# Kernel tuning notes

Hardware: AMD Instinct MI355X
Metric: run time of the kernel (lower is better)

## Reference

```python
import jax, jax.numpy as jnp
import numpy as np

NUM_OBJ = 32
OBJ_DIM = 128
MSG_W = 256
FIN_W = 256
BATCH = 256
BN_EPS = 1e-5
NEG_SLOPE = 0.01


def _linear_init(key, fan_in, fan_out):
    # torch nn.Linear default: U(-1/sqrt(fan_in), 1/sqrt(fan_in))
    kw, kb = jax.random.split(key)
    bound = 1.0 / np.sqrt(fan_in)
    w = jax.random.uniform(kw, (fan_out, fan_in), jnp.float32, -bound, bound)
    b = jax.random.uniform(kb, (fan_out,), jnp.float32, -bound, bound)
    return w, b


def setup_inputs() -> dict:
    key = jax.random.key(0)
    ks = jax.random.split(key, 8)
    state = jax.random.normal(ks[0], (BATCH, NUM_OBJ, OBJ_DIM), jnp.float32)
    edges = jax.random.randint(ks[1], (BATCH, NUM_OBJ * NUM_OBJ), 0, 2).astype(jnp.float32)
    msg_w1, msg_b1 = _linear_init(ks[2], OBJ_DIM * 2, MSG_W)
    msg_w2, msg_b2 = _linear_init(ks[3], MSG_W, OBJ_DIM)
    fin_w1, fin_b1 = _linear_init(ks[4], OBJ_DIM * 2, FIN_W)
    fin_w2, fin_b2 = _linear_init(ks[5], FIN_W, OBJ_DIM)
    msg_gamma = jnp.ones((MSG_W,), jnp.float32)
    msg_beta = jnp.zeros((MSG_W,), jnp.float32)
    fin_gamma = jnp.ones((FIN_W,), jnp.float32)
    fin_beta = jnp.zeros((FIN_W,), jnp.float32)
    return {
        "state": state, "edges": edges,
        "msg_w1": msg_w1, "msg_b1": msg_b1, "msg_gamma": msg_gamma, "msg_beta": msg_beta,
        "msg_w2": msg_w2, "msg_b2": msg_b2,
        "fin_w1": fin_w1, "fin_b1": fin_b1, "fin_gamma": fin_gamma, "fin_beta": fin_beta,
        "fin_w2": fin_w2, "fin_b2": fin_b2,
    }


def _batchnorm_train(x, gamma, beta):
    # training-mode BatchNorm1d: batch stats over rows, biased variance
    mean = jnp.mean(x, axis=0)
    var = jnp.mean(jnp.square(x - mean), axis=0)
    return (x - mean) * jax.lax.rsqrt(var + BN_EPS) * gamma + beta


def _mlp(x, w1, b1, gamma, beta, w2, b2):
    h = x @ w1.T + b1
    h = _batchnorm_train(h, gamma, beta)
    h = jnp.where(h >= 0, h, NEG_SLOPE * h)  # LeakyReLU
    return h @ w2.T + b2


def reference(state, edges, msg_w1, msg_b1, msg_gamma, msg_beta, msg_w2, msg_b2,
              fin_w1, fin_b1, fin_gamma, fin_beta, fin_w2, fin_b2):
    B, n, d = state.shape
    src = jnp.repeat(jnp.arange(n), n)   # [n*n]
    tgt = jnp.tile(jnp.arange(n), n)     # [n*n]
    sources = state[:, src]              # [B, n*n, d]
    targets = state[:, tgt]              # [B, n*n, d]
    e = edges[:, :, None]                # [B, n*n, 1]
    need = jnp.concatenate([sources * e, targets * e], axis=2)  # [B, n*n, 2d]
    msgs = _mlp(need.reshape(-1, 2 * d), msg_w1, msg_b1, msg_gamma, msg_beta, msg_w2, msg_b2)
    agg = jnp.sum(msgs.reshape(B, n, n, d), axis=2)  # sum over inner edge group
    sm = jnp.concatenate([state, agg], axis=2).reshape(-1, 2 * d)
    out = _mlp(sm, fin_w1, fin_b1, fin_gamma, fin_beta, fin_w2, fin_b2)
    return out.reshape(B, n, d)
```

## Files before the change

kernel.cpp:

```cpp
#include <hip/hip_runtime.h>

#define NOBJ   32
#define DIM    128
#define HW     256
#define R1     8192
#define NPAIR  262144
#define BN_EPS 1e-5f

typedef unsigned short u16;
typedef unsigned int   u32;
typedef __attribute__((ext_vector_type(8))) short bf16x8;
typedef __attribute__((ext_vector_type(4))) float f32x4;
typedef __attribute__((ext_vector_type(4))) unsigned short u16x4;
typedef __attribute__((ext_vector_type(4))) unsigned int u32x4;

__device__ __forceinline__ u16 f2bf(float f) {
    union { float f; unsigned u; } v; v.f = f;
    unsigned r = v.u + 0x7fffu + ((v.u >> 16) & 1u);
    return (u16)(r >> 16);
}
__device__ __forceinline__ float bf2f(u16 u) {
    union { unsigned u; float f; } v; v.u = ((unsigned)u) << 16; return v.f;
}
__device__ __forceinline__ u16x4 cvt4(float4 v) {
    u16x4 r;
    r[0] = f2bf(v.x); r[1] = f2bf(v.y); r[2] = f2bf(v.z); r[3] = f2bf(v.w);
    return r;
}
__device__ __forceinline__ bf16x8 cvt8_f32(const float* p) {
    f32x4 v0 = *(const f32x4*)p, v1 = *(const f32x4*)(p + 4);
    bf16x8 r;
    #pragma unroll
    for (int k = 0; k < 4; ++k) {
        r[k]     = (short)f2bf(v0[k]);
        r[4 + k] = (short)f2bf(v1[k]);
    }
    return r;
}
__device__ __forceinline__ bf16x8 cvt8_bn_b(const u16* p, const float* a, const float* d) {
    u16x4 v0 = *(const u16x4*)p, v1 = *(const u16x4*)(p + 4);
    f32x4 a0 = *(const f32x4*)a, a1 = *(const f32x4*)(a + 4);
    f32x4 d0 = *(const f32x4*)d, d1 = *(const f32x4*)(d + 4);
    bf16x8 r;
    #pragma unroll
    for (int k = 0; k < 4; ++k) {
        float x0 = fmaf(a0[k], bf2f(v0[k]), d0[k]); x0 = fmaxf(x0, 0.01f * x0);
        float x1 = fmaf(a1[k], bf2f(v1[k]), d1[k]); x1 = fmaxf(x1, 0.01f * x1);
        r[k]     = (short)f2bf(x0);
        r[4 + k] = (short)f2bf(x1);
    }
    return r;
}

__global__ __launch_bounds__(256) void prep_kernel(
    const float* __restrict__ w1, const float4* __restrict__ w2,
    const float4* __restrict__ fw1, const float4* __restrict__ fw2,
    u16x4* __restrict__ W1b, u16x4* __restrict__ W2b,
    u16x4* __restrict__ FW1b, u16x4* __restrict__ FW2b,
    f32x4* __restrict__ sums)
{
    int g = blockIdx.x * 256 + threadIdx.x;
    if (g < 16384) {
        const int o = g * 4, n = o >> 7, k = o & 127;
        const float4 v = *(const float4*)(w1 + (n < 256 ? n * 256 + k
                                                        : (n - 256) * 256 + 128 + k));
        W1b[g] = cvt4(v); return;
    }
    g -= 16384;
    if (g < 8192) { W2b[g] = cvt4(w2[g]); return; }
    g -= 8192;
    if (g < 16384) { FW1b[g] = cvt4(fw1[g]); return; }
    g -= 16384;
    if (g < 8192) { FW2b[g] = cvt4(fw2[g]); return; }
    g -= 8192;
    if (g < 264) { const f32x4 z = {}; sums[g] = z; }
}

__global__ __launch_bounds__(1024) void pq_stats(
    const float* __restrict__ state, const u16* __restrict__ W1b,
    const float* __restrict__ edges, const float* __restrict__ b1,
    u16* __restrict__ PQb, u16* __restrict__ Ab, float* __restrict__ EQf,
    float* __restrict__ sums)
{
    __shared__ float Qls[33 * 256];
    __shared__ float redA[16 * 256];
    __shared__ float redB[16 * 256];
    __shared__ u32 masks[32];
    __shared__ __align__(16) unsigned char list8[32 * 32];
    __shared__ float cdf[32];

    const int b    = blockIdx.x;
    const int t    = threadIdx.x;
    const int lane = t & 63;
    const int w    = t >> 6;
    const int lr   = lane & 15;
    const int lk   = (lane >> 4) * 8;
    const int c0   = lane * 4;

    if (t < 256) ((u32*)list8)[t] = 0x20202020u;
    if (t < 64) { const f32x4 z = {}; *(f32x4*)&Qls[32 * 256 + t * 4] = z; }

    const float ev = edges[(size_t)b * 1024 + t];

    const int col0 = w * 32;
    f32x4 acc[2][2] = {};
    #pragma unroll
    for (int ks = 0; ks < 4; ++ks) {
        const int kabs = ks * 32 + lk;
        bf16x8 af[2];
        #pragma unroll
        for (int rf = 0; rf < 2; ++rf)
            af[rf] = cvt8_f32(state + (size_t)(b * 32 + rf * 16 + lr) * 128 + kabs);
        if (w == 0) {
            #pragma unroll
            for (int rf = 0; rf < 2; ++rf)
                *(bf16x8*)(Ab + (size_t)(b * 32 + rf * 16 + lr) * 128 + kabs) = af[rf];
        }
        #pragma unroll
        for (int cf = 0; cf < 2; ++cf) {
            const bf16x8 bf = *(const bf16x8*)(W1b + (size_t)(col0 + cf * 16 + lr) * 128 + kabs);
            #pragma unroll
            for (int rf = 0; rf < 2; ++rf)
                acc[rf][cf] = __builtin_amdgcn_mfma_f32_16x16x32_bf16(af[rf], bf, acc[rf][cf], 0, 0, 0);
        }
    }
    #pragma unroll
    for (int rf = 0; rf < 2; ++rf)
        #pragma unroll
        for (int cf = 0; cf < 2; ++cf) {
            const int col = col0 + cf * 16 + lr;
            #pragma unroll
            for (int r = 0; r < 4; ++r) {
                const int row = rf * 16 + (lane >> 4) * 4 + r;
                const u16 u = f2bf(acc[rf][cf][r]);
                PQb[(size_t)(b * 32 + row) * 512 + col] = u;
                if (col >= 256) Qls[row * 256 + (col - 256)] = bf2f(u);
            }
        }
    __syncthreads();

    {
        const int il_t = t >> 5;
        const int j_t  = t & 31;
        const unsigned long long bal = __ballot(ev != 0.f);
        const u32 m32 = (lane < 32) ? (u32)bal : (u32)(bal >> 32);
        if (ev != 0.f)
            list8[il_t * 32 + __popc(m32 & ((1u << j_t) - 1u))] = (unsigned char)j_t;
        if (j_t == 0) masks[il_t] = m32;
    }
    __syncthreads();

    if (t < 32) {
        u32 cnt = 0;
        #pragma unroll
        for (int i = 0; i < 32; ++i) cnt += (masks[i] >> t) & 1u;
        cdf[t] = (float)cnt;
    }
    if (t == 0) {
        int tot = 0;
        #pragma unroll
        for (int i = 0; i < 32; ++i) tot += __popc(masks[i]);
        atomicAdd(&sums[512], (float)tot);
    }

    const f32x4 b14 = *(const f32x4*)(b1 + c0);
    f32x4 sumA = {}, sumB = {};

    #pragma unroll
    for (int ii = 0; ii < 2; ++ii) {
        const int il = 2 * w + ii;
        const int n1 = __popc(masks[il]);
        const int npad = (n1 + 3) & ~3;
        const float frd = (float)n1;
        f32x4 eq = {};
        const u32x4 l0 = *(const u32x4*)(list8 + il * 32);
        const u32x4 l1 = *(const u32x4*)(list8 + il * 32 + 16);
        const u32 wbuf[8] = {l0[0], l0[1], l0[2], l0[3], l1[0], l1[1], l1[2], l1[3]};
        #pragma unroll
        for (int wi = 0; wi < 8; ++wi) {
            if (wi * 4 >= npad) break;
            const u32 w4 = wbuf[wi];
            #pragma unroll
            for (int kb = 0; kb < 4; ++kb) {
                const int j = (w4 >> (kb * 8)) & 0xff;
                const f32x4 q = *(const f32x4*)&Qls[j * 256 + c0];
                #pragma unroll
                for (int k = 0; k < 4; ++k) eq[k] += q[k];
            }
        }
        *(f32x4*)(EQf + (size_t)(b * 32 + il) * 256 + c0) = eq;
        const u16x4 pu = *(const u16x4*)(PQb + (size_t)(b * 32 + il) * 512 + c0);
        #pragma unroll
        for (int k = 0; k < 4; ++k) {
            const float pb = bf2f(pu[k]) + b14[k];
            sumA[k] += frd * pb + eq[k];
            sumB[k] = fmaf(frd * pb + 2.f * eq[k], pb, sumB[k]);
        }
    }
    __syncthreads();

    #pragma unroll
    for (int jj = 0; jj < 2; ++jj) {
        const int j = 2 * w + jj;
        const float cdj = cdf[j];
        const f32x4 q = *(const f32x4*)&Qls[j * 256 + c0];
        #pragma unroll
        for (int k = 0; k < 4; ++k) sumB[k] = fmaf(cdj * q[k], q[k], sumB[k]);
    }
    *(f32x4*)&redA[w * 256 + c0] = sumA;
    *(f32x4*)&redB[w * 256 + c0] = sumB;
    __syncthreads();
    if (t < 256) {
        float a = 0.f, bb = 0.f;
        #pragma unroll
        for (int ww = 0; ww < 16; ++ww) {
            a  += redA[ww * 256 + t];
            bb += redB[ww * 256 + t];
        }
        atomicAdd(&sums[t], a);
        atomicAdd(&sums[256 + t], bb);
    }
}

__global__ __launch_bounds__(512) void s_agg_kernel(
    const u16* __restrict__ PQb, const float* __restrict__ edges,
    const float* __restrict__ EQf, const float* __restrict__ sums,
    const float* __restrict__ gamma, const float* __restrict__ beta,
    const float* __restrict__ b1,
    const u16* __restrict__ W2b, const float* __restrict__ b2,
    u16* __restrict__ aggb)
{
    __shared__ float Qls[33 * 256];
    __shared__ u16 Ssb[16 * 256];
    __shared__ __align__(16) unsigned char list8[16 * 32];
    __shared__ int n1s[16];

    const int b    = blockIdx.x;
    const int i0   = blockIdx.y * 16;
    const int t    = threadIdx.x;
    const int lane = t & 63;
    const int w    = t >> 6;
    const int lr   = lane & 15;
    const int lk   = (lane >> 4) * 8;
    const int c0   = lane * 4;

    const float Etot = sums[512];
    const float nz   = (float)NPAIR - Etot;
    const float invN = 1.f / (float)NPAIR;
    const f32x4 s1  = *(const f32x4*)(sums + c0);
    const f32x4 s2  = *(const f32x4*)(sums + 256 + c0);
    const f32x4 g4  = *(const f32x4*)(gamma + c0);
    const f32x4 be4 = *(const f32x4*)(beta + c0);
    const f32x4 b14 = *(const f32x4*)(b1 + c0);
    f32x4 a4, d4, ld4;
    #pragma unroll
    for (int k = 0; k < 4; ++k) {
        const float mean = (s1[k] + nz * b14[k]) * invN;
        const float ms   = (s2[k] + nz * b14[k] * b14[k]) * invN;
        const float var  = fmaf(-mean, mean, ms);
        a4[k]  = g4[k] * rsqrtf(var + BN_EPS);
        d4[k]  = fmaf(b14[k] - mean, a4[k], be4[k]);
        ld4[k] = fmaxf(d4[k], 0.01f * d4[k]);
    }

    #pragma unroll
    for (int it = 0; it < 4; ++it) {
        const int row = w + it * 8;
        const u16x4 qu = *(const u16x4*)(PQb + (size_t)(b * 32 + row) * 512 + 256 + c0);
        f32x4 q;
        #pragma unroll
        for (int k = 0; k < 4; ++k) q[k] = a4[k] * bf2f(qu[k]);
        *(f32x4*)&Qls[row * 256 + c0] = q;
    }
    if (t < 64) { const f32x4 z = {}; *(f32x4*)&Qls[32 * 256 + t * 4] = z; }
    if (t < 128) ((u32*)list8)[t] = 0x20202020u;

    const float ev = edges[(size_t)b * 1024 + (i0 + (t >> 5)) * 32 + (t & 31)];
    __syncthreads();

    {
        const int il_t = t >> 5;
        const int j_t  = t & 31;
        const unsigned long long bal = __ballot(ev != 0.f);
        const u32 m32 = (lane < 32) ? (u32)bal : (u32)(bal >> 32);
        if (ev != 0.f)
            list8[il_t * 32 + __popc(m32 & ((1u << j_t) - 1u))] = (unsigned char)j_t;
        if (j_t == 0) n1s[il_t] = __popc(m32);
    }
    __syncthreads();

    #pragma unroll
    for (int ii = 0; ii < 2; ++ii) {
        const int il = 2 * w + ii;
        const int gi = b * 32 + i0 + il;
        const int n1 = n1s[il];
        const int npad = (n1 + 3) & ~3;
        const float frd = (float)n1;
        const float fz = (float)(32 - n1);
        const float fp = (float)(npad - n1);
        const u16x4 pu = *(const u16x4*)(PQb + (size_t)gi * 512 + c0);
        const f32x4 eq4 = *(const f32x4*)(EQf + (size_t)gi * 256 + c0);
        f32x4 ap, absacc;
        #pragma unroll
        for (int k = 0; k < 4; ++k) {
            ap[k] = fmaf(a4[k], bf2f(pu[k]), d4[k]);
            absacc[k] = -fp * fabsf(ap[k]);
        }
        const u32x4 l0 = *(const u32x4*)(list8 + il * 32);
        const u32x4 l1 = *(const u32x4*)(list8 + il * 32 + 16);
        const u32 wbuf[8] = {l0[0], l0[1], l0[2], l0[3], l1[0], l1[1], l1[2], l1[3]};
        #pragma unroll
        for (int wi = 0; wi < 8; ++wi) {
            if (wi * 4 >= npad) break;
            const u32 w4 = wbuf[wi];
            #pragma unroll
            for (int kb = 0; kb < 4; ++kb) {
                const int j = (w4 >> (kb * 8)) & 0xff;
                const f32x4 q = *(const f32x4*)&Qls[j * 256 + c0];
                #pragma unroll
                for (int k = 0; k < 4; ++k)
                    absacc[k] += fabsf(ap[k] + q[k]);
            }
        }
        u16x4 o;
        #pragma unroll
        for (int k = 0; k < 4; ++k) {
            const float lin = fmaf(frd, ap[k], a4[k] * eq4[k]);
            const float S = fmaf(fz, ld4[k], fmaf(0.505f, lin, 0.495f * absacc[k]));
            o[k] = f2bf(S);
        }
        const int off = (lane * 8) ^ ((il & 7) << 4);
        *(u16x4*)((char*)Ssb + il * 512 + off) = o;
    }
    __syncthreads();

    const int colw = w * 16;
    f32x4 acc2 = {};
    #pragma unroll
    for (int ks = 0; ks < 8; ++ks) {
        const int rdoff = (ks * 64 + (lane >> 4) * 16) ^ ((lr & 7) << 4);
        const bf16x8 afr = *(const bf16x8*)((const char*)Ssb + lr * 512 + rdoff);
        const bf16x8 bfr = *(const bf16x8*)(W2b + (size_t)(colw + lr) * 256 + ks * 32 + lk);
        acc2 = __builtin_amdgcn_mfma_f32_16x16x32_bf16(afr, bfr, acc2, 0, 0, 0);
    }
    {
        const int col = colw + lr;
        const float bv = (float)NOBJ * b2[col];
        #pragma unroll
        for (int r = 0; r < 4; ++r) {
            const int rowl = (lane >> 4) * 4 + r;
            aggb[(size_t)(b * 32 + i0 + rowl) * 128 + col] = f2bf(acc2[r] + bv);
        }
    }
}

__global__ __launch_bounds__(256) void h2_gemm(
    const u16* __restrict__ Ab, const u16* __restrict__ aggb,
    const u16* __restrict__ FW1b, const float* __restrict__ fb1,
    u16* __restrict__ H2b, float* __restrict__ sums2)
{
    __shared__ float sred[64];
    const int lane = threadIdx.x & 63;
    const int wave = threadIdx.x >> 6;
    const int row0 = blockIdx.y * 64 + wave * 16;
    const int col0 = blockIdx.x * 32;
    const int lr = lane & 15;
    const int lk = (lane >> 4) * 8;

    f32x4 acc[2] = {};
    #pragma unroll
    for (int ks = 0; ks < 8; ++ks) {
        const int kabs = ks * 32 + lk;
        const bf16x8 af = (kabs < 128)
            ? *(const bf16x8*)(Ab   + (size_t)(row0 + lr) * 128 + kabs)
            : *(const bf16x8*)(aggb + (size_t)(row0 + lr) * 128 + (kabs - 128));
        #pragma unroll
        for (int cf = 0; cf < 2; ++cf) {
            const bf16x8 bf = *(const bf16x8*)(FW1b + (size_t)(col0 + cf * 16 + lr) * 256 + kabs);
            acc[cf] = __builtin_amdgcn_mfma_f32_16x16x32_bf16(af, bf, acc[cf], 0, 0, 0);
        }
    }

    if (threadIdx.x < 64) sred[threadIdx.x] = 0.f;
    __syncthreads();
    #pragma unroll
    for (int cf = 0; cf < 2; ++cf) {
        const int col = col0 + cf * 16 + lr;
        const float bv = fb1[col];
        float s = 0.f, ss = 0.f;
        #pragma unroll
        for (int r = 0; r < 4; ++r) {
            const int row = row0 + (lane >> 4) * 4 + r;
            const float v = acc[cf][r] + bv;
            H2b[(size_t)row * 256 + col] = f2bf(v);
            s += v;
            ss = fmaf(v, v, ss);
        }
        atomicAdd(&sred[cf * 16 + lr], s);
        atomicAdd(&sred[32 + cf * 16 + lr], ss);
    }
    __syncthreads();
    if (threadIdx.x < 32) {
        atomicAdd(&sums2[col0 + threadIdx.x], sred[threadIdx.x]);
        atomicAdd(&sums2[256 + col0 + threadIdx.x], sred[32 + threadIdx.x]);
    }
}

__global__ __launch_bounds__(256) void out_gemm(
    const u16* __restrict__ H2b, const u16* __restrict__ FW2b,
    const float* __restrict__ fb2, const float* __restrict__ sums2,
    const float* __restrict__ gamma, const float* __restrict__ beta,
    float* __restrict__ out)
{
    __shared__ float adl[512];
    const int t = threadIdx.x;
    {
        const float invN = 1.f / (float)R1;
        const float mean = sums2[t] * invN;
        const float var  = fmaf(-mean, mean, sums2[256 + t] * invN);
        const float a    = gamma[t] * rsqrtf(var + BN_EPS);
        adl[t]       = a;
        adl[256 + t] = fmaf(-mean, a, beta[t]);
    }
    __syncthreads();

    const int lane = t & 63;
    const int wave = t >> 6;
    const int row0 = blockIdx.y * 64 + wave * 16;
    const int col0 = blockIdx.x * 32;
    const int lr = lane & 15;
    const int lk = (lane >> 4) * 8;

    f32x4 acc[2] = {};
    #pragma unroll
    for (int ks = 0; ks < 8; ++ks) {
        const int kabs = ks * 32 + lk;
        const bf16x8 af = cvt8_bn_b(H2b + (size_t)(row0 + lr) * 256 + kabs,
                                    adl + kabs, adl + 256 + kabs);
        #pragma unroll
        for (int cf = 0; cf < 2; ++cf) {
            const bf16x8 bf = *(const bf16x8*)(FW2b + (size_t)(col0 + cf * 16 + lr) * 256 + kabs);
            acc[cf] = __builtin_amdgcn_mfma_f32_16x16x32_bf16(af, bf, acc[cf], 0, 0, 0);
        }
    }
    #pragma unroll
    for (int cf = 0; cf < 2; ++cf) {
        const int col = col0 + cf * 16 + lr;
        const float bv = fb2[col];
        #pragma unroll
        for (int r = 0; r < 4; ++r) {
            const int row = row0 + (lane >> 4) * 4 + r;
            out[(size_t)row * 128 + col] = acc[cf][r] + bv;
        }
    }
}

extern "C" void kernel_launch(void* const* d_in, const int* in_sizes, int n_in,
                              void* d_out, int out_size, void* d_ws, size_t ws_size,
                              hipStream_t stream)
{
    const float* state     = (const float*)d_in[0];
    const float* edges     = (const float*)d_in[1];
    const float* msg_w1    = (const float*)d_in[2];
    const float* msg_b1    = (const float*)d_in[3];
    const float* msg_gamma = (const float*)d_in[4];
    const float* msg_beta  = (const float*)d_in[5];
    const float* msg_w2    = (const float*)d_in[6];
    const float* msg_b2    = (const float*)d_in[7];
    const float* fin_w1    = (const float*)d_in[8];
    const float* fin_b1    = (const float*)d_in[9];
    const float* fin_gamma = (const float*)d_in[10];
    const float* fin_beta  = (const float*)d_in[11];
    const float* fin_w2    = (const float*)d_in[12];
    const float* fin_b2    = (const float*)d_in[13];

    char* w = (char*)d_ws;
    u16*   PQb  = (u16*)(w);
    u16*   Ab   = (u16*)(w + 8388608);
    u16*   aggb = (u16*)(w + 10485760);
    u16*   H2b  = (u16*)(w + 12582912);
    float* EQf  = (float*)(w + 16777216);
    u16*   W1b  = (u16*)(w + 25165824);
    u16*   W2b  = (u16*)(w + 25296896);
    u16*   FW1b = (u16*)(w + 25362432);
    u16*   FW2b = (u16*)(w + 25493504);
    float* sums = (float*)(w + 25559040);
    float* sums2 = sums + 544;

    prep_kernel<<<195, 256, 0, stream>>>(
        msg_w1, (const float4*)msg_w2, (const float4*)fin_w1, (const float4*)fin_w2,
        (u16x4*)W1b, (u16x4*)W2b, (u16x4*)FW1b, (u16x4*)FW2b, (f32x4*)sums);

    pq_stats<<<256, 1024, 0, stream>>>(state, W1b, edges, msg_b1,
                                       PQb, Ab, EQf, sums);

    s_agg_kernel<<<dim3(256, 2), 512, 0, stream>>>(
        PQb, edges, EQf, sums, msg_gamma, msg_beta, msg_b1, W2b, msg_b2, aggb);

    h2_gemm<<<dim3(8, 128), 256, 0, stream>>>(Ab, aggb, FW1b, fin_b1, H2b, sums2);

    out_gemm<<<dim3(4, 128), 256, 0, stream>>>(
        H2b, FW2b, fin_b2, sums2, fin_gamma, fin_beta, (float*)d_out);
}
```

Baseline: 69.09 us.

## Fuse h2 GEMM into aggregation kernel and drop weight-conversion prep kernel

```diff
diff --git a/kernel.cpp b/kernel.cpp
--- a/kernel.cpp
+++ b/kernel.cpp
@@ -1,9 +1,5 @@
 #include <hip/hip_runtime.h>
 
-#define NOBJ   32
-#define DIM    128
-#define HW     256
-#define R1     8192
 #define NPAIR  262144
 #define BN_EPS 1e-5f
 
@@ -22,11 +18,6 @@
 __device__ __forceinline__ float bf2f(u16 u) {
     union { unsigned u; float f; } v; v.u = ((unsigned)u) << 16; return v.f;
 }
-__device__ __forceinline__ u16x4 cvt4(float4 v) {
-    u16x4 r;
-    r[0] = f2bf(v.x); r[1] = f2bf(v.y); r[2] = f2bf(v.z); r[3] = f2bf(v.w);
-    return r;
-}
 __device__ __forceinline__ bf16x8 cvt8_f32(const float* p) {
     f32x4 v0 = *(const f32x4*)p, v1 = *(const f32x4*)(p + 4);
     bf16x8 r;
@@ -52,34 +43,10 @@
     return r;
 }
 
-__global__ __launch_bounds__(256) void prep_kernel(
-    const float* __restrict__ w1, const float4* __restrict__ w2,
-    const float4* __restrict__ fw1, const float4* __restrict__ fw2,
-    u16x4* __restrict__ W1b, u16x4* __restrict__ W2b,
-    u16x4* __restrict__ FW1b, u16x4* __restrict__ FW2b,
-    f32x4* __restrict__ sums)
-{
-    int g = blockIdx.x * 256 + threadIdx.x;
-    if (g < 16384) {
-        const int o = g * 4, n = o >> 7, k = o & 127;
-        const float4 v = *(const float4*)(w1 + (n < 256 ? n * 256 + k
-                                                        : (n - 256) * 256 + 128 + k));
-        W1b[g] = cvt4(v); return;
-    }
-    g -= 16384;
-    if (g < 8192) { W2b[g] = cvt4(w2[g]); return; }
-    g -= 8192;
-    if (g < 16384) { FW1b[g] = cvt4(fw1[g]); return; }
-    g -= 16384;
-    if (g < 8192) { FW2b[g] = cvt4(fw2[g]); return; }
-    g -= 8192;
-    if (g < 264) { const f32x4 z = {}; sums[g] = z; }
-}
-
 __global__ __launch_bounds__(1024) void pq_stats(
-    const float* __restrict__ state, const u16* __restrict__ W1b,
+    const float* __restrict__ state, const float* __restrict__ w1,
     const float* __restrict__ edges, const float* __restrict__ b1,
-    u16* __restrict__ PQb, u16* __restrict__ Ab, float* __restrict__ EQf,
+    u16* __restrict__ PQb, float* __restrict__ EQf,
     float* __restrict__ sums)
 {
     __shared__ float Qls[33 * 256];
@@ -111,17 +78,15 @@
         #pragma unroll
         for (int rf = 0; rf < 2; ++rf)
             af[rf] = cvt8_f32(state + (size_t)(b * 32 + rf * 16 + lr) * 128 + kabs);
-        if (w == 0) {
+        #pragma unroll
+        for (int cf = 0; cf < 2; ++cf) {
+            const int coln = col0 + cf * 16 + lr;
+            const float* wp = (coln < 256) ? (w1 + (size_t)coln * 256 + kabs)
+                                           : (w1 + (size_t)(coln - 256) * 256 + 128 + kabs);
+            const bf16x8 bfr = cvt8_f32(wp);
             #pragma unroll
             for (int rf = 0; rf < 2; ++rf)
-                *(bf16x8*)(Ab + (size_t)(b * 32 + rf * 16 + lr) * 128 + kabs) = af[rf];
-        }
-        #pragma unroll
-        for (int cf = 0; cf < 2; ++cf) {
-            const bf16x8 bf = *(const bf16x8*)(W1b + (size_t)(col0 + cf * 16 + lr) * 128 + kabs);
-            #pragma unroll
-            for (int rf = 0; rf < 2; ++rf)
-                acc[rf][cf] = __builtin_amdgcn_mfma_f32_16x16x32_bf16(af[rf], bf, acc[rf][cf], 0, 0, 0);
+                acc[rf][cf] = __builtin_amdgcn_mfma_f32_16x16x32_bf16(af[rf], bfr, acc[rf][cf], 0, 0, 0);
         }
     }
     #pragma unroll
@@ -222,18 +187,22 @@
     }
 }
 
-__global__ __launch_bounds__(512) void s_agg_kernel(
+__global__ __launch_bounds__(512) void s_agg_h2_kernel(
     const u16* __restrict__ PQb, const float* __restrict__ edges,
     const float* __restrict__ EQf, const float* __restrict__ sums,
     const float* __restrict__ gamma, const float* __restrict__ beta,
-    const float* __restrict__ b1,
-    const u16* __restrict__ W2b, const float* __restrict__ b2,
-    u16* __restrict__ aggb)
+    const float* __restrict__ b1, const float* __restrict__ state,
+    const float* __restrict__ w2, const float* __restrict__ b2,
+    const float* __restrict__ fw1, const float* __restrict__ fb1,
+    u16* __restrict__ H2b, float* __restrict__ sums2)
 {
     __shared__ float Qls[33 * 256];
     __shared__ u16 Ssb[16 * 256];
+    __shared__ u16 Asb[16 * 128];
+    __shared__ u16 aggs[16 * 128];
     __shared__ __align__(16) unsigned char list8[16 * 32];
     __shared__ int n1s[16];
+    __shared__ float sred[512];
 
     const int b    = blockIdx.x;
     const int i0   = blockIdx.y * 16;
@@ -241,8 +210,11 @@
     const int lane = t & 63;
     const int w    = t >> 6;
     const int lr   = lane & 15;
-    const int lk   = (lane >> 4) * 8;
+    const int lkg  = lane >> 4;
+    const int lk   = lkg * 8;
     const int c0   = lane * 4;
+
+    sred[t] = 0.f;
 
     const float Etot = sums[512];
     const float nz   = (float)NPAIR - Etot;
@@ -271,6 +243,11 @@
         #pragma unroll
         for (int k = 0; k < 4; ++k) q[k] = a4[k] * bf2f(qu[k]);
         *(f32x4*)&Qls[row * 256 + c0] = q;
+    }
+    if (t < 256) {
+        const int row = t >> 4, k8 = (t & 15) * 8;
+        const bf16x8 av = cvt8_f32(state + (size_t)(b * 32 + i0 + row) * 128 + k8);
+        *(bf16x8*)((char*)Asb + ((row * 256 + k8 * 2) ^ ((row & 7) << 4))) = av;
     }
     if (t < 64) { const f32x4 z = {}; *(f32x4*)&Qls[32 * 256 + t * 4] = z; }
     if (t < 128) ((u32*)list8)[t] = 0x20202020u;
@@ -329,85 +306,73 @@
             const float S = fmaf(fz, ld4[k], fmaf(0.505f, lin, 0.495f * absacc[k]));
             o[k] = f2bf(S);
         }
-        const int off = (lane * 8) ^ ((il & 7) << 4);
-        *(u16x4*)((char*)Ssb + il * 512 + off) = o;
-    }
-    __syncthreads();
-
-    const int colw = w * 16;
-    f32x4 acc2 = {};
-    #pragma unroll
-    for (int ks = 0; ks < 8; ++ks) {
-        const int rdoff = (ks * 64 + (lane >> 4) * 16) ^ ((lr & 7) << 4);
-        const bf16x8 afr = *(const bf16x8*)((const char*)Ssb + lr * 512 + rdoff);
-        const bf16x8 bfr = *(const bf16x8*)(W2b + (size_t)(colw + lr) * 256 + ks * 32 + lk);
-        acc2 = __builtin_amdgcn_mfma_f32_16x16x32_bf16(afr, bfr, acc2, 0, 0, 0);
-    }
+        *(u16x4*)((char*)Ssb + il * 512 + ((lane * 8) ^ ((il & 7) << 4))) = o;
+    }
+    __syncthreads();
+
     {
-        const int col = colw + lr;
-        const float bv = (float)NOBJ * b2[col];
+        f32x4 acc2 = {};
+        #pragma unroll
+        for (int ks = 0; ks < 8; ++ks) {
+            const int rdoff = (ks * 64 + lkg * 16) ^ ((lr & 7) << 4);
+            const bf16x8 afr = *(const bf16x8*)((const char*)Ssb + lr * 512 + rdoff);
+            const bf16x8 bfr = cvt8_f32(w2 + (size_t)(w * 16 + lr) * 256 + ks * 32 + lk);
+            acc2 = __builtin_amdgcn_mfma_f32_16x16x32_bf16(afr, bfr, acc2, 0, 0, 0);
+        }
+        const int col = w * 16 + lr;
+        const float bv = 32.f * b2[col];
         #pragma unroll
         for (int r = 0; r < 4; ++r) {
-            const int rowl = (lane >> 4) * 4 + r;
-            aggb[(size_t)(b * 32 + i0 + rowl) * 128 + col] = f2bf(acc2[r] + bv);
-        }
-    }
-}
-
-__global__ __launch_bounds__(256) void h2_gemm(
-    const u16* __restrict__ Ab, const u16* __restrict__ aggb,
-    const u16* __restrict__ FW1b, const float* __restrict__ fb1,
-    u16* __restrict__ H2b, float* __restrict__ sums2)
-{
-    __shared__ float sred[64];
-    const int lane = threadIdx.x & 63;
-    const int wave = threadIdx.x >> 6;
-    const int row0 = blockIdx.y * 64 + wave * 16;
-    const int col0 = blockIdx.x * 32;
-    const int lr = lane & 15;
-    const int lk = (lane >> 4) * 8;
-
-    f32x4 acc[2] = {};
-    #pragma unroll
-    for (int ks = 0; ks < 8; ++ks) {
-        const int kabs = ks * 32 + lk;
-        const bf16x8 af = (kabs < 128)
-            ? *(const bf16x8*)(Ab   + (size_t)(row0 + lr) * 128 + kabs)
-            : *(const bf16x8*)(aggb + (size_t)(row0 + lr) * 128 + (kabs - 128));
+            const int row = lkg * 4 + r;
+            *(u16*)((char*)aggs + ((row * 256 + col * 2) ^ ((row & 7) << 4))) = f2bf(acc2[r] + bv);
+        }
+    }
+    __syncthreads();
+
+    {
+        f32x4 acc3[2] = {};
+        #pragma unroll
+        for (int ks = 0; ks < 8; ++ks) {
+            const int kabs = ks * 32 + lk;
+            const int row = lr;
+            bf16x8 af3;
+            if (ks < 4)
+                af3 = *(const bf16x8*)((const char*)Asb + ((row * 256 + kabs * 2) ^ ((row & 7) << 4)));
+            else
+                af3 = *(const bf16x8*)((const char*)aggs + ((row * 256 + (kabs - 128) * 2) ^ ((row & 7) << 4)));
+            #pragma unroll
+            for (int cf = 0; cf < 2; ++cf) {
+                const int col = w * 32 + cf * 16 + lr;
+                const bf16x8 bfr = cvt8_f32(fw1 + (size_t)col * 256 + kabs);
+                acc3[cf] = __builtin_amdgcn_mfma_f32_16x16x32_bf16(af3, bfr, acc3[cf], 0, 0, 0);
+            }
+        }
         #pragma unroll
         for (int cf = 0; cf < 2; ++cf) {
-            const bf16x8 bf = *(const bf16x8*)(FW1b + (size_t)(col0 + cf * 16 + lr) * 256 + kabs);
-            acc[cf] = __builtin_amdgcn_mfma_f32_16x16x32_bf16(af, bf, acc[cf], 0, 0, 0);
-        }
-    }
-
-    if (threadIdx.x < 64) sred[threadIdx.x] = 0.f;
-    __syncthreads();
-    #pragma unroll
-    for (int cf = 0; cf < 2; ++cf) {
-        const int col = col0 + cf * 16 + lr;
-        const float bv = fb1[col];
-        float s = 0.f, ss = 0.f;
-        #pragma unroll
-        for (int r = 0; r < 4; ++r) {
-            const int row = row0 + (lane >> 4) * 4 + r;
-            const float v = acc[cf][r] + bv;
-            H2b[(size_t)row * 256 + col] = f2bf(v);
-            s += v;
-            ss = fmaf(v, v, ss);
-        }
-        atomicAdd(&sred[cf * 16 + lr], s);
-        atomicAdd(&sred[32 + cf * 16 + lr], ss);
-    }
-    __syncthreads();
-    if (threadIdx.x < 32) {
-        atomicAdd(&sums2[col0 + threadIdx.x], sred[threadIdx.x]);
-        atomicAdd(&sums2[256 + col0 + threadIdx.x], sred[32 + threadIdx.x]);
+            const int col = w * 32 + cf * 16 + lr;
+            const float bv = fb1[col];
+            float s = 0.f, ss = 0.f;
+            #pragma unroll
+            for (int r = 0; r < 4; ++r) {
+                const int row = lkg * 4 + r;
+                const float v = acc3[cf][r] + bv;
+                H2b[(size_t)(b * 32 + i0 + row) * 256 + col] = f2bf(v);
+                s += v;
+                ss = fmaf(v, v, ss);
+            }
+            atomicAdd(&sred[col], s);
+            atomicAdd(&sred[256 + col], ss);
+        }
+    }
+    __syncthreads();
+    if (t < 256) {
+        atomicAdd(&sums2[t], sred[t]);
+        atomicAdd(&sums2[256 + t], sred[256 + t]);
     }
 }
 
 __global__ __launch_bounds__(256) void out_gemm(
-    const u16* __restrict__ H2b, const u16* __restrict__ FW2b,
+    const u16* __restrict__ H2b, const float* __restrict__ fw2,
     const float* __restrict__ fb2, const float* __restrict__ sums2,
     const float* __restrict__ gamma, const float* __restrict__ beta,
     float* __restrict__ out)
@@ -415,9 +380,9 @@
     __shared__ float adl[512];
     const int t = threadIdx.x;
     {
-        const float invN = 1.f / (float)R1;
-        const float mean = sums2[t] * invN;
-        const float var  = fmaf(-mean, mean, sums2[256 + t] * invN);
+        const float invR = 1.f / 8192.f;
+        const float mean = sums2[t] * invR;
+        const float var  = fmaf(-mean, mean, sums2[256 + t] * invR);
         const float a    = gamma[t] * rsqrtf(var + BN_EPS);
         adl[t]       = a;
         adl[256 + t] = fmaf(-mean, a, beta[t]);
@@ -439,7 +404,7 @@
                                     adl + kabs, adl + 256 + kabs);
         #pragma unroll
         for (int cf = 0; cf < 2; ++cf) {
-            const bf16x8 bf = *(const bf16x8*)(FW2b + (size_t)(col0 + cf * 16 + lr) * 256 + kabs);
+            const bf16x8 bf = cvt8_f32(fw2 + (size_t)(col0 + cf * 16 + lr) * 256 + kabs);
             acc[cf] = __builtin_amdgcn_mfma_f32_16x16x32_bf16(af, bf, acc[cf], 0, 0, 0);
         }
     }
@@ -476,29 +441,20 @@
 
     char* w = (char*)d_ws;
     u16*   PQb  = (u16*)(w);
-    u16*   Ab   = (u16*)(w + 8388608);
-    u16*   aggb = (u16*)(w + 10485760);
-    u16*   H2b  = (u16*)(w + 12582912);
-    float* EQf  = (float*)(w + 16777216);
-    u16*   W1b  = (u16*)(w + 25165824);
-    u16*   W2b  = (u16*)(w + 25296896);
-    u16*   FW1b = (u16*)(w + 25362432);
-    u16*   FW2b = (u16*)(w + 25493504);
-    float* sums = (float*)(w + 25559040);
+    float* EQf  = (float*)(w + 8388608);
+    u16*   H2b  = (u16*)(w + 16777216);
+    float* sums = (float*)(w + 20971520);
     float* sums2 = sums + 544;
 
-    prep_kernel<<<195, 256, 0, stream>>>(
-        msg_w1, (const float4*)msg_w2, (const float4*)fin_w1, (const float4*)fin_w2,
-        (u16x4*)W1b, (u16x4*)W2b, (u16x4*)FW1b, (u16x4*)FW2b, (f32x4*)sums);
-
-    pq_stats<<<256, 1024, 0, stream>>>(state, W1b, edges, msg_b1,
-                                       PQb, Ab, EQf, sums);
-
-    s_agg_kernel<<<dim3(256, 2), 512, 0, stream>>>(
-        PQb, edges, EQf, sums, msg_gamma, msg_beta, msg_b1, W2b, msg_b2, aggb);
-
-    h2_gemm<<<dim3(8, 128), 256, 0, stream>>>(Ab, aggb, FW1b, fin_b1, H2b, sums2);
+    hipMemsetAsync(sums, 0, 1088 * sizeof(float), stream);
+
+    pq_stats<<<256, 1024, 0, stream>>>(state, msg_w1, edges, msg_b1,
+                                       PQb, EQf, sums);
+
+    s_agg_h2_kernel<<<dim3(256, 2), 512, 0, stream>>>(
+        PQb, edges, EQf, sums, msg_gamma, msg_beta, msg_b1,
+        state, msg_w2, msg_b2, fin_w1, fin_b1, H2b, sums2);
 
     out_gemm<<<dim3(4, 128), 256, 0, stream>>>(
-        H2b, FW2b, fin_b2, sums2, fin_gamma, fin_beta, (float*)d_out);
-}
+        H2b, fin_w2, fin_b2, sums2, fin_gamma, fin_beta, (float*)d_out);
+}
```

Result: slower. 82.93 us (+20.0%).
